# Kernel optimization log

Hardware: AMD Instinct MI355X
Metric: run time of the kernel (lower is better)

## Reference

```python
import jax, jax.numpy as jnp
import numpy as np

N = 10000      # nodes
E = 100000     # edges
C = 32         # in_channels == hidden_channels == out_channels
ED = 4         # edge_dim
G = 64         # number of graphs in the batch
EPS = 1e-5     # BatchNorm eps


def setup_inputs() -> dict:
    key = jax.random.key(0)
    ks = jax.random.split(key, 20)
    rn = lambda k, shape, s=0.05: jax.random.normal(k, shape, dtype=jnp.float32) * s
    return {
        "x": jax.random.normal(ks[0], (N, C), dtype=jnp.float32),
        "edge_attr": jax.random.normal(ks[1], (E, ED), dtype=jnp.float32),
        # edge MLP 1: ED -> C -> C*C ; NNConv1 root/bias
        "e1_w1": rn(ks[2], (ED, C)), "e1_b1": jnp.zeros((C,), jnp.float32),
        "e1_w2": rn(ks[3], (C, C * C)), "e1_b2": jnp.zeros((C * C,), jnp.float32),
        "root1": rn(ks[4], (C, C)), "bias1": jnp.zeros((C,), jnp.float32),
        # edge MLP 2: ED -> C -> C*C ; NNConv2 root/bias
        "e2_w1": rn(ks[5], (ED, C)), "e2_b1": jnp.zeros((C,), jnp.float32),
        "e2_w2": rn(ks[6], (C, C * C)), "e2_b2": jnp.zeros((C * C,), jnp.float32),
        "root2": rn(ks[7], (C, C)), "bias2": jnp.zeros((C,), jnp.float32),
        # BatchNorm (eval mode: running stats)
        "bn1_g": jnp.ones((C,), jnp.float32), "bn1_b": jnp.zeros((C,), jnp.float32),
        "bn1_m": rn(ks[8], (C,), 0.1), "bn1_v": 1.0 + 0.1 * jax.random.uniform(ks[9], (C,), dtype=jnp.float32),
        "bn2_g": jnp.ones((C,), jnp.float32), "bn2_b": jnp.zeros((C,), jnp.float32),
        "bn2_m": rn(ks[10], (C,), 0.1), "bn2_v": 1.0 + 0.1 * jax.random.uniform(ks[11], (C,), dtype=jnp.float32),
        # readout: C -> C//2 -> 1
        "r1_w": rn(ks[12], (C, C // 2)), "r1_b": jnp.zeros((C // 2,), jnp.float32),
        "r2_w": rn(ks[13], (C // 2, 1)), "r2_b": jnp.zeros((1,), jnp.float32),
        "edge_index": jax.random.randint(ks[14], (2, E), 0, N),
        "batch": jnp.sort(jax.random.randint(ks[15], (N,), 0, G)),
    }


def _nnconv(x, edge_index, edge_attr, w1, b1, w2, b2, root, bias):
    # edge MLP -> per-edge weight matrix [E, C, C]
    h = jax.nn.relu(edge_attr @ w1 + b1)
    W = (h @ w2 + b2).reshape(E, C, C)
    src, dst = edge_index[0], edge_index[1]
    # gather source features, per-edge matmul, scatter-mean to target nodes
    msg = jnp.einsum('ei,eio->eo', x[src], W)                      # [E, C]
    agg = jax.ops.segment_sum(msg, dst, num_segments=N)            # [N, C]
    cnt = jax.ops.segment_sum(jnp.ones((E,), x.dtype), dst, num_segments=N)
    agg = agg / jnp.maximum(cnt, 1.0)[:, None]
    return agg + x @ root + bias


def _bn(x, g, b, m, v):
    return (x - m) * jax.lax.rsqrt(v + EPS) * g + b


def reference(x, edge_attr,
              e1_w1, e1_b1, e1_w2, e1_b2, root1, bias1,
              e2_w1, e2_b1, e2_w2, e2_b2, root2, bias2,
              bn1_g, bn1_b, bn1_m, bn1_v,
              bn2_g, bn2_b, bn2_m, bn2_v,
              r1_w, r1_b, r2_w, r2_b,
              edge_index, batch):
    h = jax.nn.relu(_bn(_nnconv(x, edge_index, edge_attr, e1_w1, e1_b1, e1_w2, e1_b2, root1, bias1),
                        bn1_g, bn1_b, bn1_m, bn1_v))
    h = jax.nn.relu(_bn(_nnconv(h, edge_index, edge_attr, e2_w1, e2_b1, e2_w2, e2_b2, root2, bias2),
                        bn2_g, bn2_b, bn2_m, bn2_v))
    # global mean pool over graphs
    psum = jax.ops.segment_sum(h, batch, num_segments=G)           # [G, C]
    pcnt = jax.ops.segment_sum(jnp.ones((N,), h.dtype), batch, num_segments=G)
    pooled = psum / jnp.maximum(pcnt, 1.0)[:, None]
    # readout MLP (dropout is identity in eval)
    return jax.nn.relu(pooled @ r1_w + r1_b) @ r2_w + r2_b          # [G, 1]
```

## Files before the change

kernel.cpp:

```cpp
#include <hip/hip_runtime.h>

#define NN 10000
#define EE 100000
#define CC 32
#define GG 64
#define EPSV 1e-5f
#define NB 8
#define SLOTS 1056
#define PST 36
#define PNODE (32*PST)
#define HBLK ((EE+255)/256)
#define WBLK 160

__global__ __launch_bounds__(256) void k_pre(const int* __restrict__ ei,
        int* __restrict__ cnt, int* __restrict__ deg,
        const float* __restrict__ w2a, const float* __restrict__ b2a,
        const float* __restrict__ w2b, const float* __restrict__ b2b,
        float* __restrict__ w2r1, float* __restrict__ w2r2) {
    int blk = blockIdx.x;
    int t = threadIdx.x;
    if (blk < HBLK) {
        int e = blk * 256 + t;
        if (e < EE) {
            atomicAdd(&cnt[ei[EE + e]], 1);
            atomicAdd(&deg[ei[e]], 1);
        }
    } else {
        int b2i = blk - HBLK;
        int s = (b2i % 5) * 256 + t;
        int i = b2i / 5;
        if (s < SLOTS) {
            float va = (s < 1024) ? w2a[(s >> 5) * 1024 + i * 32 + (s & 31)]
                                  : b2a[i * 32 + (s - 1024)];
            float vb = (s < 1024) ? w2b[(s >> 5) * 1024 + i * 32 + (s & 31)]
                                  : b2b[i * 32 + (s - 1024)];
            w2r1[i * SLOTS + s] = va;
            w2r2[i * SLOTS + s] = vb;
        }
    }
}

__global__ __launch_bounds__(1024) void k_scan(const int* __restrict__ deg,
                                               const int* __restrict__ cnt,
                                               int* __restrict__ rowptr,
                                               int* __restrict__ cursor,
                                               int* __restrict__ colptr,
                                               int* __restrict__ ccursor) {
    __shared__ int buf[1024];
    int t = threadIdx.x;
    int base = t * 10;
    for (int pass = 0; pass < 2; pass++) {
        const int* src = pass ? cnt : deg;
        int* dst_p = pass ? colptr : rowptr;
        int* dst_c = pass ? ccursor : cursor;
        int v[10]; int s = 0;
        #pragma unroll
        for (int k = 0; k < 10; k++) {
            int idx = base + k;
            v[k] = (idx < NN) ? src[idx] : 0;
            s += v[k];
        }
        buf[t] = s;
        for (int off = 1; off < 1024; off <<= 1) {
            __syncthreads();
            int val = buf[t] + ((t >= off) ? buf[t - off] : 0);
            __syncthreads();
            buf[t] = val;
        }
        __syncthreads();
        int carry = (t > 0) ? buf[t - 1] : 0;
        #pragma unroll
        for (int k = 0; k < 10; k++) {
            int idx = base + k;
            if (idx < NN) { dst_p[idx] = carry; dst_c[idx] = carry; }
            carry += v[k];
        }
        if (t == 1023) dst_p[NN] = buf[1023];
        __syncthreads();
    }
}

__global__ void k_scatter(const int* __restrict__ ei,
        const float* __restrict__ edge_attr,
        int* __restrict__ cursor, int* __restrict__ ccursor,
        int* __restrict__ msrc, int* __restrict__ cpos,
        float4* __restrict__ ea_csr) {
    int e = blockIdx.x * 256 + threadIdx.x;
    if (e >= EE) return;
    int sn = ei[e];
    int dn = ei[EE + e];
    float4 a = *(const float4*)&edge_attr[(size_t)e * 4];
    int pos = atomicAdd(&cursor[sn], 1);
    msrc[pos] = sn;
    ea_csr[pos] = a;
    int cp = atomicAdd(&ccursor[dn], 1);
    cpos[cp] = pos;
}

__global__ __launch_bounds__(256, 3) void k_fused3(const float* __restrict__ x,
        const float4* __restrict__ ea_csr,
        const float* __restrict__ w1, const float* __restrict__ b1,
        const float* __restrict__ w2r,
        const int* __restrict__ msrc, const int* __restrict__ rowptr,
        float* __restrict__ msg) {
    __shared__ float xs[NB][32];
    __shared__ float P2[NB * PNODE];
    __shared__ float shx[8][32];
    int t = threadIdx.x;
    int o = t & 31;
    int cb = 4 * (t >> 5);
    int n0 = blockIdx.x * NB;

    int ebase = rowptr[n0];
    int eend  = rowptr[n0 + NB];
    int grp = t >> 5;

    float wc0 = w1[o], wc1 = w1[32 + o], wc2 = w1[64 + o], wc3 = w1[96 + o];
    float bb  = b1[o];

    int pos = ebase + grp;
    float4 aC = make_float4(0.f, 0.f, 0.f, 0.f);
    int srcC = n0;
    if (pos < eend) {
        aC = ea_csr[pos];
        srcC = msrc[pos];
    }

    xs[t >> 5][t & 31] = x[n0 * 32 + t];
    __syncthreads();

    {
        float acc[4][NB];
        #pragma unroll
        for (int k = 0; k < 4; k++)
            #pragma unroll
            for (int n = 0; n < NB; n++) acc[k][n] = 0.f;
        #pragma unroll
        for (int j = 0; j < 8; j++) {
            float wk[4][4];
            #pragma unroll
            for (int r = 0; r < 4; r++)
                #pragma unroll
                for (int k = 0; k < 4; k++)
                    wk[r][k] = w2r[(4 * j + r) * SLOTS + (cb + k) * 32 + o];
            #pragma unroll
            for (int n = 0; n < NB; n++) {
                float4 xq = *(const float4*)&xs[n][4 * j];
                #pragma unroll
                for (int k = 0; k < 4; k++)
                    acc[k][n] += xq.x * wk[0][k] + xq.y * wk[1][k]
                               + xq.z * wk[2][k] + xq.w * wk[3][k];
            }
        }
        #pragma unroll
        for (int n = 0; n < NB; n++) {
            float4 st = make_float4(acc[0][n], acc[1][n], acc[2][n], acc[3][n]);
            *(float4*)&P2[n * PNODE + o * PST + cb] = st;
        }
    }
    if (t < 32) {
        float wb[32];
        #pragma unroll
        for (int i = 0; i < 32; i++) wb[i] = w2r[i * SLOTS + 1024 + t];
        #pragma unroll
        for (int n = 0; n < NB; n++) {
            float b = 0.f;
            #pragma unroll
            for (int j = 0; j < 8; j++) {
                float4 xq = *(const float4*)&xs[n][4 * j];
                b += xq.x * wb[4 * j] + xq.y * wb[4 * j + 1]
                   + xq.z * wb[4 * j + 2] + xq.w * wb[4 * j + 3];
            }
            *(float4*)&P2[n * PNODE + t * PST + 32] = make_float4(b, 0.f, 0.f, 0.f);
        }
    }
    __syncthreads();

    while (pos < eend) {
        int pn = pos + 8;
        float4 aN = aC; int srcN = srcC;
        if (pn < eend) {
            aN = ea_csr[pn];
            srcN = msrc[pn];
        }
        float h = fmaxf(aC.x * wc0 + aC.y * wc1 + aC.z * wc2 + aC.w * wc3 + bb, 0.f);
        shx[grp][o] = h;
        asm volatile("" ::: "memory");
        const float* Pn = &P2[(srcC - n0) * PNODE + o * PST];
        float m = Pn[32];
        #pragma unroll
        for (int b = 0; b < 8; b++) {
            float4 hx = *(const float4*)&shx[grp][4 * b];
            float4 pq = *(const float4*)&Pn[4 * b];
            m += hx.x * pq.x + hx.y * pq.y + hx.z * pq.z + hx.w * pq.w;
        }
        msg[(size_t)pos * 32 + o] = m;
        asm volatile("" ::: "memory");
        pos = pn; aC = aN; srcC = srcN;
    }
}

__global__ __launch_bounds__(256) void k_combine(const float* __restrict__ x_in,
        const float* __restrict__ msg,
        const int* __restrict__ colptr, const int* __restrict__ cpos,
        const float* __restrict__ root, const float* __restrict__ bias,
        const float* __restrict__ bng, const float* __restrict__ bnb,
        const float* __restrict__ bnm, const float* __restrict__ bnv,
        float* __restrict__ x_out, float* __restrict__ psum,
        const int* __restrict__ batch) {
    __shared__ float xs[8][32];
    __shared__ float vals[8][32];
    __shared__ int gb[8];
    int t = threadIdx.x;
    int n0 = blockIdx.x * 8;
    xs[t >> 5][t & 31] = x_in[n0 * 32 + t];
    __syncthreads();
    int k = t >> 5, o = t & 31, n = n0 + k;
    float r = bias[o];
    #pragma unroll
    for (int i = 0; i < 32; i++) r += xs[k][i] * root[i * 32 + o];
    int jbase = colptr[n], jend = colptr[n + 1];
    float acc = 0.f;
    for (int jb = jbase; jb < jend; jb += 32) {
        int nrem = jend - jb;
        int lim = (nrem < 32) ? nrem : 32;
        int cv = 0;
        if (o < lim) cv = cpos[jb + o];
        for (int j = 0; j < lim; j += 8) {
            float v[8];
            #pragma unroll
            for (int q = 0; q < 8; q++) {
                if (j + q < lim) {
                    int cj = __shfl(cv, j + q, 32);
                    v[q] = msg[(size_t)cj * 32 + o];
                } else v[q] = 0.f;
            }
            #pragma unroll
            for (int q = 0; q < 8; q++) acc += v[q];
        }
    }
    float a = acc / fmaxf((float)(jend - jbase), 1.f);
    float val = a + r;
    val = (val - bnm[o]) * rsqrtf(bnv[o] + EPSV) * bng[o] + bnb[o];
    val = fmaxf(val, 0.f);
    if (x_out) {
        x_out[(size_t)n * 32 + o] = val;
    }
    if (psum) {
        vals[k][o] = val;
        if (o == 0) gb[k] = batch[n];
        __syncthreads();
        if (k == 0) {
            float pacc = vals[0][o];
            int g = gb[0];
            #pragma unroll
            for (int k2 = 1; k2 < 8; k2++) {
                if (gb[k2] == g) pacc += vals[k2][o];
                else {
                    atomicAdd(&psum[(size_t)g * 32 + o], pacc);
                    g = gb[k2]; pacc = vals[k2][o];
                }
            }
            atomicAdd(&psum[(size_t)g * 32 + o], pacc);
        }
    }
}

__global__ __launch_bounds__(256) void k_readout(const float* __restrict__ psum,
        const int* __restrict__ batch,
        const float* __restrict__ r1w, const float* __restrict__ r1b,
        const float* __restrict__ r2w, const float* __restrict__ r2b,
        float* __restrict__ out) {
    __shared__ float w1s[32 * 16];
    __shared__ float b1s[16];
    __shared__ float w2s[16];
    __shared__ float ps[GG * 32];
    int t = threadIdx.x;
    int cnt_g = 0;
    if (t < GG) {
        int lo = 0, hi = NN;
        while (lo < hi) { int m = (lo + hi) >> 1; if (batch[m] < t) lo = m + 1; else hi = m; }
        int lb = lo;
        lo = 0; hi = NN;
        while (lo < hi) { int m = (lo + hi) >> 1; if (batch[m] < t + 1) lo = m + 1; else hi = m; }
        cnt_g = lo - lb;
    }
    w1s[t] = r1w[t];
    w1s[t + 256] = r1w[t + 256];
    if (t < 16) { b1s[t] = r1b[t]; w2s[t] = r2w[t]; }
    #pragma unroll
    for (int i = 0; i < GG * 32 / 256; i++) ps[t + i * 256] = psum[t + i * 256];
    __syncthreads();
    if (t < GG) {
        float inv = 1.f / fmaxf((float)cnt_g, 1.f);
        float acc = r2b[0];
        #pragma unroll
        for (int j = 0; j < 16; j++) {
            float dot = 0.f;
            #pragma unroll
            for (int c = 0; c < 32; c++) dot += ps[t * 32 + c] * w1s[c * 16 + j];
            float z = dot * inv + b1s[j];
            acc += fmaxf(z, 0.f) * w2s[j];
        }
        out[t] = acc;
    }
}

extern "C" void kernel_launch(void* const* d_in, const int* in_sizes, int n_in,
                              void* d_out, int out_size, void* d_ws, size_t ws_size,
                              hipStream_t stream) {
    const float* x       = (const float*)d_in[0];
    const float* eattr   = (const float*)d_in[1];
    const float* e1_w1   = (const float*)d_in[2];
    const float* e1_b1   = (const float*)d_in[3];
    const float* e1_w2   = (const float*)d_in[4];
    const float* e1_b2   = (const float*)d_in[5];
    const float* root1   = (const float*)d_in[6];
    const float* bias1   = (const float*)d_in[7];
    const float* e2_w1   = (const float*)d_in[8];
    const float* e2_b1   = (const float*)d_in[9];
    const float* e2_w2   = (const float*)d_in[10];
    const float* e2_b2   = (const float*)d_in[11];
    const float* root2   = (const float*)d_in[12];
    const float* bias2   = (const float*)d_in[13];
    const float* bn1_g   = (const float*)d_in[14];
    const float* bn1_b   = (const float*)d_in[15];
    const float* bn1_m   = (const float*)d_in[16];
    const float* bn1_v   = (const float*)d_in[17];
    const float* bn2_g   = (const float*)d_in[18];
    const float* bn2_b   = (const float*)d_in[19];
    const float* bn2_m   = (const float*)d_in[20];
    const float* bn2_v   = (const float*)d_in[21];
    const float* r1_w    = (const float*)d_in[22];
    const float* r1_b    = (const float*)d_in[23];
    const float* r2_w    = (const float*)d_in[24];
    const float* r2_b    = (const float*)d_in[25];
    const int*   ei      = (const int*)d_in[26];
    const int*   batch   = (const int*)d_in[27];

    char* ws = (char*)d_ws;
    float*  w2r1   = (float*) (ws);
    float*  w2r2   = (float*) (ws + 135168);
    float*  msg    = (float*) (ws + 270336);
    float4* ea_csr = (float4*)(ws + 13070336);
    int*    cnt    = (int*)   (ws + 14670336);
    int*    deg    = (int*)   (ws + 14710336);
    float*  psum   = (float*) (ws + 14750336);
    float*  xmid   = (float*) (ws + 14758528);
    int*    rowptr = (int*)   (ws + 16038528);
    int*    cursor = (int*)   (ws + 16078592);
    int*    colptr = (int*)   (ws + 16118592);
    int*    ccursor= (int*)   (ws + 16158656);
    int*    msrc   = (int*)   (ws + 16198656);
    int*    cpos   = (int*)   (ws + 16598656);

    hipMemsetAsync(ws + 14670336, 0, 88192, stream);

    k_pre<<<HBLK + WBLK, 256, 0, stream>>>(ei, cnt, deg,
                                           e1_w2, e1_b2, e2_w2, e2_b2, w2r1, w2r2);
    k_scan<<<1, 1024, 0, stream>>>(deg, cnt, rowptr, cursor, colptr, ccursor);
    k_scatter<<<(EE + 255) / 256, 256, 0, stream>>>(ei, eattr,
                                                    cursor, ccursor, msrc, cpos,
                                                    ea_csr);

    k_fused3<<<NN / NB, 256, 0, stream>>>(x, ea_csr, e1_w1, e1_b1, w2r1,
                                          msrc, rowptr, msg);
    k_combine<<<NN / 8, 256, 0, stream>>>(x, msg, colptr, cpos, root1, bias1,
                                          bn1_g, bn1_b, bn1_m, bn1_v,
                                          xmid, nullptr, batch);

    k_fused3<<<NN / NB, 256, 0, stream>>>(xmid, ea_csr, e2_w1, e2_b1, w2r2,
                                          msrc, rowptr, msg);
    k_combine<<<NN / 8, 256, 0, stream>>>(xmid, msg, colptr, cpos, root2, bias2,
                                          bn2_g, bn2_b, bn2_m, bn2_v,
                                          nullptr, psum, batch);

    k_readout<<<1, 256, 0, stream>>>(psum, batch, r1_w, r1_b, r2_w, r2_b, (float*)d_out);
}
```

Measured before the change: 255.0 us.

## Fuse all stages into one persistent kernel with software grid barriers

Replaces eight separate kernel launches and a memset with a single 625-block persistent kernel that uses atomic-counter grid barriers between phases: degree counting, scan, CSR scatter, two message/combine layers, and readout. The layer-1 output stays in shared memory for each block's 16 nodes instead of going through global memory, and the two layers write to separate message buffers. The intent is to remove launch overhead and inter-kernel gaps. In exchange it depends on all 625 blocks being co-resident, otherwise the spin barriers deadlock. The scan and readout phases also run on only one or two blocks while the rest wait.

```diff
diff --git a/kernel.cpp b/kernel.cpp
--- a/kernel.cpp
+++ b/kernel.cpp
@@ -2,66 +2,129 @@
 
 #define NN 10000
 #define EE 100000
-#define CC 32
 #define GG 64
 #define EPSV 1e-5f
-#define NB 8
+#define NBLK 625
+#define NPB 16
 #define SLOTS 1056
 #define PST 36
 #define PNODE (32*PST)
-#define HBLK ((EE+255)/256)
+#define HBLK 391
 #define WBLK 160
 
-__global__ __launch_bounds__(256) void k_pre(const int* __restrict__ ei,
-        int* __restrict__ cnt, int* __restrict__ deg,
-        const float* __restrict__ w2a, const float* __restrict__ b2a,
-        const float* __restrict__ w2b, const float* __restrict__ b2b,
-        float* __restrict__ w2r1, float* __restrict__ w2r2) {
-    int blk = blockIdx.x;
-    int t = threadIdx.x;
-    if (blk < HBLK) {
-        int e = blk * 256 + t;
-        if (e < EE) {
-            atomicAdd(&cnt[ei[EE + e]], 1);
-            atomicAdd(&deg[ei[e]], 1);
-        }
-    } else {
-        int b2i = blk - HBLK;
+#define OFF_W2R1   0
+#define OFF_W2R2   135168
+#define OFF_MSG1   270336
+#define OFF_MSG2   13070336
+#define OFF_EACSR  25870336
+#define OFF_CNT    27470336
+#define OFF_DEG    27510336
+#define OFF_PSUM   27550336
+#define OFF_ROWPTR 27558528
+#define OFF_CURSOR 27598592
+#define OFF_COLPTR 27638592
+#define OFF_CCUR   27678656
+#define OFF_MSRC   27718656
+#define OFF_CPOS   28118656
+#define OFF_BARS   28518656
+
+__device__ __forceinline__ void gsync(int* bars, int slot) {
+    __syncthreads();
+    if (threadIdx.x == 0) {
+        __threadfence();
+        int base = atomicAdd(&bars[slot], 1);
+        int target = (base / NBLK + 1) * NBLK;
+        while (__hip_atomic_load(&bars[slot], __ATOMIC_RELAXED,
+                                 __HIP_MEMORY_SCOPE_AGENT) < target)
+            __builtin_amdgcn_s_sleep(2);
+        __threadfence();
+    }
+    __syncthreads();
+}
+
+__global__ __launch_bounds__(256, 3) void k_mega(
+    const float* __restrict__ x, const float* __restrict__ eattr,
+    const float* __restrict__ e1w1, const float* __restrict__ e1b1,
+    const float* __restrict__ e2w1, const float* __restrict__ e2b1,
+    const float* __restrict__ e1w2, const float* __restrict__ e1b2,
+    const float* __restrict__ e2w2, const float* __restrict__ e2b2,
+    const float* __restrict__ root1, const float* __restrict__ bias1,
+    const float* __restrict__ root2, const float* __restrict__ bias2,
+    const float* __restrict__ bn1g, const float* __restrict__ bn1b,
+    const float* __restrict__ bn1m, const float* __restrict__ bn1v,
+    const float* __restrict__ bn2g, const float* __restrict__ bn2b,
+    const float* __restrict__ bn2m, const float* __restrict__ bn2v,
+    const float* __restrict__ r1w, const float* __restrict__ r1b,
+    const float* __restrict__ r2w, const float* __restrict__ r2b,
+    const int* __restrict__ ei, const int* __restrict__ batch,
+    float* __restrict__ out, char* __restrict__ ws)
+{
+    __shared__ float xs[8][32];
+    __shared__ float P2[8 * PNODE];
+    __shared__ float shx[8][32];
+    __shared__ float xmid_s[NPB][32];
+
+    float*  w2r1   = (float*) (ws + OFF_W2R1);
+    float*  w2r2   = (float*) (ws + OFF_W2R2);
+    float*  msg1   = (float*) (ws + OFF_MSG1);
+    float*  msg2   = (float*) (ws + OFF_MSG2);
+    float4* ea_csr = (float4*)(ws + OFF_EACSR);
+    int*    cnt    = (int*)   (ws + OFF_CNT);
+    int*    deg    = (int*)   (ws + OFF_DEG);
+    float*  psum   = (float*) (ws + OFF_PSUM);
+    int*    rowptr = (int*)   (ws + OFF_ROWPTR);
+    int*    cursor = (int*)   (ws + OFF_CURSOR);
+    int*    colptr = (int*)   (ws + OFF_COLPTR);
+    int*    ccursor= (int*)   (ws + OFF_CCUR);
+    int*    msrc   = (int*)   (ws + OFF_MSRC);
+    int*    cpos   = (int*)   (ws + OFF_CPOS);
+    int*    bars   = (int*)   (ws + OFF_BARS);
+
+    int bid  = blockIdx.x;
+    int t    = threadIdx.x;
+    int gtid = bid * 256 + t;
+    int o    = t & 31;
+    int grp  = t >> 5;
+
+    if (gtid < NN) { cnt[gtid] = 0; deg[gtid] = 0; }
+    if (gtid < GG * 32) psum[gtid] = 0.f;
+    if (bid >= HBLK && bid < HBLK + WBLK) {
+        int b2i = bid - HBLK;
         int s = (b2i % 5) * 256 + t;
         int i = b2i / 5;
         if (s < SLOTS) {
-            float va = (s < 1024) ? w2a[(s >> 5) * 1024 + i * 32 + (s & 31)]
-                                  : b2a[i * 32 + (s - 1024)];
-            float vb = (s < 1024) ? w2b[(s >> 5) * 1024 + i * 32 + (s & 31)]
-                                  : b2b[i * 32 + (s - 1024)];
+            float va = (s < 1024) ? e1w2[(s >> 5) * 1024 + i * 32 + (s & 31)]
+                                  : e1b2[i * 32 + (s - 1024)];
+            float vb = (s < 1024) ? e2w2[(s >> 5) * 1024 + i * 32 + (s & 31)]
+                                  : e2b2[i * 32 + (s - 1024)];
             w2r1[i * SLOTS + s] = va;
             w2r2[i * SLOTS + s] = vb;
         }
     }
-}
-
-__global__ __launch_bounds__(1024) void k_scan(const int* __restrict__ deg,
-                                               const int* __restrict__ cnt,
-                                               int* __restrict__ rowptr,
-                                               int* __restrict__ cursor,
-                                               int* __restrict__ colptr,
-                                               int* __restrict__ ccursor) {
-    __shared__ int buf[1024];
-    int t = threadIdx.x;
-    int base = t * 10;
-    for (int pass = 0; pass < 2; pass++) {
-        const int* src = pass ? cnt : deg;
-        int* dst_p = pass ? colptr : rowptr;
-        int* dst_c = pass ? ccursor : cursor;
-        int v[10]; int s = 0;
+    gsync(bars, 0);
+
+    if (gtid < EE) {
+        atomicAdd(&cnt[ei[EE + gtid]], 1);
+        atomicAdd(&deg[ei[gtid]], 1);
+    }
+    gsync(bars, 1);
+
+    if (bid < 2) {
+        const int* srcv = bid ? cnt : deg;
+        int* dp = bid ? colptr : rowptr;
+        int* dc = bid ? ccursor : cursor;
+        int* buf = (int*)xs;
+        int vloc[40];
+        int ssum = 0;
+        int base = t * 40;
         #pragma unroll
-        for (int k = 0; k < 10; k++) {
+        for (int k = 0; k < 40; k++) {
             int idx = base + k;
-            v[k] = (idx < NN) ? src[idx] : 0;
-            s += v[k];
-        }
-        buf[t] = s;
-        for (int off = 1; off < 1024; off <<= 1) {
+            vloc[k] = (idx < NN) ? srcv[idx] : 0;
+            ssum += vloc[k];
+        }
+        buf[t] = ssum;
+        for (int off = 1; off < 256; off <<= 1) {
             __syncthreads();
             int val = buf[t] + ((t >= off) ? buf[t - off] : 0);
             __syncthreads();
@@ -70,239 +133,219 @@
         __syncthreads();
         int carry = (t > 0) ? buf[t - 1] : 0;
         #pragma unroll
-        for (int k = 0; k < 10; k++) {
+        for (int k = 0; k < 40; k++) {
             int idx = base + k;
-            if (idx < NN) { dst_p[idx] = carry; dst_c[idx] = carry; }
-            carry += v[k];
-        }
-        if (t == 1023) dst_p[NN] = buf[1023];
+            if (idx < NN) { dp[idx] = carry; dc[idx] = carry; }
+            carry += vloc[k];
+        }
+        if (t == 255) dp[NN] = buf[255];
+    }
+    gsync(bars, 2);
+
+    if (gtid < EE) {
+        int sn = ei[gtid];
+        int dn = ei[EE + gtid];
+        float4 a = *(const float4*)&eattr[(size_t)gtid * 4];
+        int pos = atomicAdd(&cursor[sn], 1);
+        msrc[pos] = sn;
+        ea_csr[pos] = a;
+        int cp = atomicAdd(&ccursor[dn], 1);
+        cpos[cp] = pos;
+    }
+    gsync(bars, 3);
+
+    for (int layer = 0; layer < 2; ++layer) {
+        const float* w2r  = layer ? w2r2 : w2r1;
+        const float* w1   = layer ? e2w1 : e1w1;
+        const float* b1   = layer ? e2b1 : e1b1;
+        float*       msgL = layer ? msg2 : msg1;
+        const float* root = layer ? root2 : root1;
+        const float* bias = layer ? bias2 : bias1;
+        const float* bg   = layer ? bn2g : bn1g;
+        const float* bbn  = layer ? bn2b : bn1b;
+        const float* bm   = layer ? bn2m : bn1m;
+        const float* bv   = layer ? bn2v : bn1v;
+
+        float wc0 = w1[o], wc1 = w1[32 + o], wc2 = w1[64 + o], wc3 = w1[96 + o];
+        float hbb = b1[o];
+        int cb = 4 * grp;
+
+        for (int tile = 0; tile < 2; ++tile) {
+            int n0 = bid * NPB + tile * 8;
+            int ebase = rowptr[n0];
+            int eend  = rowptr[n0 + 8];
+
+            int pos = ebase + grp;
+            float4 aC = make_float4(0.f, 0.f, 0.f, 0.f);
+            int srcC = n0;
+            if (pos < eend) { aC = ea_csr[pos]; srcC = msrc[pos]; }
+
+            if (layer == 0) xs[grp][o] = x[n0 * 32 + t];
+            else            xs[grp][o] = xmid_s[tile * 8 + grp][o];
+            __syncthreads();
+
+            {
+                float acc[4][8];
+                #pragma unroll
+                for (int k = 0; k < 4; k++)
+                    #pragma unroll
+                    for (int n = 0; n < 8; n++) acc[k][n] = 0.f;
+                #pragma unroll
+                for (int j = 0; j < 8; j++) {
+                    float wk[4][4];
+                    #pragma unroll
+                    for (int r = 0; r < 4; r++)
+                        #pragma unroll
+                        for (int k = 0; k < 4; k++)
+                            wk[r][k] = w2r[(4 * j + r) * SLOTS + (cb + k) * 32 + o];
+                    #pragma unroll
+                    for (int n = 0; n < 8; n++) {
+                        float4 xq = *(const float4*)&xs[n][4 * j];
+                        #pragma unroll
+                        for (int k = 0; k < 4; k++)
+                            acc[k][n] += xq.x * wk[0][k] + xq.y * wk[1][k]
+                                       + xq.z * wk[2][k] + xq.w * wk[3][k];
+                    }
+                }
+                #pragma unroll
+                for (int n = 0; n < 8; n++) {
+                    float4 st = make_float4(acc[0][n], acc[1][n], acc[2][n], acc[3][n]);
+                    *(float4*)&P2[n * PNODE + o * PST + cb] = st;
+                }
+            }
+            if (t < 32) {
+                float wb[32];
+                #pragma unroll
+                for (int i = 0; i < 32; i++) wb[i] = w2r[i * SLOTS + 1024 + t];
+                #pragma unroll
+                for (int n = 0; n < 8; n++) {
+                    float b = 0.f;
+                    #pragma unroll
+                    for (int j = 0; j < 8; j++) {
+                        float4 xq = *(const float4*)&xs[n][4 * j];
+                        b += xq.x * wb[4 * j] + xq.y * wb[4 * j + 1]
+                           + xq.z * wb[4 * j + 2] + xq.w * wb[4 * j + 3];
+                    }
+                    *(float4*)&P2[n * PNODE + t * PST + 32] = make_float4(b, 0.f, 0.f, 0.f);
+                }
+            }
+            __syncthreads();
+
+            while (pos < eend) {
+                int pn = pos + 8;
+                float4 aN = aC; int srcN = srcC;
+                if (pn < eend) { aN = ea_csr[pn]; srcN = msrc[pn]; }
+                float h = fmaxf(aC.x * wc0 + aC.y * wc1 + aC.z * wc2 + aC.w * wc3 + hbb, 0.f);
+                shx[grp][o] = h;
+                asm volatile("" ::: "memory");
+                const float* Pn = &P2[(srcC - n0) * PNODE + o * PST];
+                float m = Pn[32];
+                #pragma unroll
+                for (int b = 0; b < 8; b++) {
+                    float4 hx = *(const float4*)&shx[grp][4 * b];
+                    float4 pq = *(const float4*)&Pn[4 * b];
+                    m += hx.x * pq.x + hx.y * pq.y + hx.z * pq.z + hx.w * pq.w;
+                }
+                msgL[(size_t)pos * 32 + o] = m;
+                asm volatile("" ::: "memory");
+                pos = pn; aC = aN; srcC = srcN;
+            }
+        }
+        gsync(bars, 4 + layer);
+
+        for (int r = 0; r < 2; ++r) {
+            __syncthreads();
+            int n0c = bid * NPB + r * 8;
+            if (layer == 0) xs[grp][o] = x[n0c * 32 + t];
+            else            xs[grp][o] = xmid_s[r * 8 + grp][o];
+            __syncthreads();
+            int k = grp, n = n0c + k;
+            float rt = bias[o];
+            #pragma unroll
+            for (int i = 0; i < 32; i++) rt += xs[k][i] * root[i * 32 + o];
+            int jbase = colptr[n], jend = colptr[n + 1];
+            float acc = 0.f;
+            for (int jb = jbase; jb < jend; jb += 32) {
+                int nrem = jend - jb;
+                int lim = (nrem < 32) ? nrem : 32;
+                int cv = 0;
+                if (o < lim) cv = cpos[jb + o];
+                for (int j = 0; j < lim; j += 8) {
+                    float v[8];
+                    #pragma unroll
+                    for (int q = 0; q < 8; q++) {
+                        if (j + q < lim) {
+                            int cj = __shfl(cv, j + q, 32);
+                            v[q] = msgL[(size_t)cj * 32 + o];
+                        } else v[q] = 0.f;
+                    }
+                    #pragma unroll
+                    for (int q = 0; q < 8; q++) acc += v[q];
+                }
+            }
+            float a = acc / fmaxf((float)(jend - jbase), 1.f);
+            float val = a + rt;
+            val = (val - bm[o]) * rsqrtf(bv[o] + EPSV) * bg[o] + bbn[o];
+            val = fmaxf(val, 0.f);
+            if (layer == 0) {
+                xmid_s[r * 8 + k][o] = val;
+            } else {
+                int* gbp = (int*)P2;
+                shx[k][o] = val;
+                if (o == 0) gbp[k] = batch[n];
+                __syncthreads();
+                if (k == 0) {
+                    float pacc = shx[0][o];
+                    int g = gbp[0];
+                    #pragma unroll
+                    for (int k2 = 1; k2 < 8; k2++) {
+                        if (gbp[k2] == g) pacc += shx[k2][o];
+                        else {
+                            atomicAdd(&psum[(size_t)g * 32 + o], pacc);
+                            g = gbp[k2]; pacc = shx[k2][o];
+                        }
+                    }
+                    atomicAdd(&psum[(size_t)g * 32 + o], pacc);
+                }
+            }
+        }
+        if (layer == 1) gsync(bars, 6);
+    }
+
+    if (bid == 0) {
         __syncthreads();
-    }
-}
-
-__global__ void k_scatter(const int* __restrict__ ei,
-        const float* __restrict__ edge_attr,
-        int* __restrict__ cursor, int* __restrict__ ccursor,
-        int* __restrict__ msrc, int* __restrict__ cpos,
-        float4* __restrict__ ea_csr) {
-    int e = blockIdx.x * 256 + threadIdx.x;
-    if (e >= EE) return;
-    int sn = ei[e];
-    int dn = ei[EE + e];
-    float4 a = *(const float4*)&edge_attr[(size_t)e * 4];
-    int pos = atomicAdd(&cursor[sn], 1);
-    msrc[pos] = sn;
-    ea_csr[pos] = a;
-    int cp = atomicAdd(&ccursor[dn], 1);
-    cpos[cp] = pos;
-}
-
-__global__ __launch_bounds__(256, 3) void k_fused3(const float* __restrict__ x,
-        const float4* __restrict__ ea_csr,
-        const float* __restrict__ w1, const float* __restrict__ b1,
-        const float* __restrict__ w2r,
-        const int* __restrict__ msrc, const int* __restrict__ rowptr,
-        float* __restrict__ msg) {
-    __shared__ float xs[NB][32];
-    __shared__ float P2[NB * PNODE];
-    __shared__ float shx[8][32];
-    int t = threadIdx.x;
-    int o = t & 31;
-    int cb = 4 * (t >> 5);
-    int n0 = blockIdx.x * NB;
-
-    int ebase = rowptr[n0];
-    int eend  = rowptr[n0 + NB];
-    int grp = t >> 5;
-
-    float wc0 = w1[o], wc1 = w1[32 + o], wc2 = w1[64 + o], wc3 = w1[96 + o];
-    float bb  = b1[o];
-
-    int pos = ebase + grp;
-    float4 aC = make_float4(0.f, 0.f, 0.f, 0.f);
-    int srcC = n0;
-    if (pos < eend) {
-        aC = ea_csr[pos];
-        srcC = msrc[pos];
-    }
-
-    xs[t >> 5][t & 31] = x[n0 * 32 + t];
-    __syncthreads();
-
-    {
-        float acc[4][NB];
+        float* w1s = P2;
+        float* b1s = P2 + 512;
+        float* w2s = P2 + 528;
+        float* ps  = P2 + 544;
+        int cnt_g = 0;
+        if (t < GG) {
+            int lo = 0, hi = NN;
+            while (lo < hi) { int m2 = (lo + hi) >> 1; if (batch[m2] < t) lo = m2 + 1; else hi = m2; }
+            int lb = lo;
+            lo = 0; hi = NN;
+            while (lo < hi) { int m2 = (lo + hi) >> 1; if (batch[m2] < t + 1) lo = m2 + 1; else hi = m2; }
+            cnt_g = lo - lb;
+        }
+        w1s[t] = r1w[t];
+        w1s[t + 256] = r1w[t + 256];
+        if (t < 16) { b1s[t] = r1b[t]; w2s[t] = r2w[t]; }
         #pragma unroll
-        for (int k = 0; k < 4; k++)
+        for (int i = 0; i < GG * 32 / 256; i++) ps[t + i * 256] = psum[t + i * 256];
+        __syncthreads();
+        if (t < GG) {
+            float inv = 1.f / fmaxf((float)cnt_g, 1.f);
+            float acc2 = r2b[0];
             #pragma unroll
-            for (int n = 0; n < NB; n++) acc[k][n] = 0.f;
-        #pragma unroll
-        for (int j = 0; j < 8; j++) {
-            float wk[4][4];
-            #pragma unroll
-            for (int r = 0; r < 4; r++)
-                #pragma unroll
-                for (int k = 0; k < 4; k++)
-                    wk[r][k] = w2r[(4 * j + r) * SLOTS + (cb + k) * 32 + o];
-            #pragma unroll
-            for (int n = 0; n < NB; n++) {
-                float4 xq = *(const float4*)&xs[n][4 * j];
-                #pragma unroll
-                for (int k = 0; k < 4; k++)
-                    acc[k][n] += xq.x * wk[0][k] + xq.y * wk[1][k]
-                               + xq.z * wk[2][k] + xq.w * wk[3][k];
-            }
-        }
-        #pragma unroll
-        for (int n = 0; n < NB; n++) {
-            float4 st = make_float4(acc[0][n], acc[1][n], acc[2][n], acc[3][n]);
-            *(float4*)&P2[n * PNODE + o * PST + cb] = st;
-        }
-    }
-    if (t < 32) {
-        float wb[32];
-        #pragma unroll
-        for (int i = 0; i < 32; i++) wb[i] = w2r[i * SLOTS + 1024 + t];
-        #pragma unroll
-        for (int n = 0; n < NB; n++) {
-            float b = 0.f;
-            #pragma unroll
-            for (int j = 0; j < 8; j++) {
-                float4 xq = *(const float4*)&xs[n][4 * j];
-                b += xq.x * wb[4 * j] + xq.y * wb[4 * j + 1]
-                   + xq.z * wb[4 * j + 2] + xq.w * wb[4 * j + 3];
-            }
-            *(float4*)&P2[n * PNODE + t * PST + 32] = make_float4(b, 0.f, 0.f, 0.f);
-        }
-    }
-    __syncthreads();
-
-    while (pos < eend) {
-        int pn = pos + 8;
-        float4 aN = aC; int srcN = srcC;
-        if (pn < eend) {
-            aN = ea_csr[pn];
-            srcN = msrc[pn];
-        }
-        float h = fmaxf(aC.x * wc0 + aC.y * wc1 + aC.z * wc2 + aC.w * wc3 + bb, 0.f);
-        shx[grp][o] = h;
-        asm volatile("" ::: "memory");
-        const float* Pn = &P2[(srcC - n0) * PNODE + o * PST];
-        float m = Pn[32];
-        #pragma unroll
-        for (int b = 0; b < 8; b++) {
-            float4 hx = *(const float4*)&shx[grp][4 * b];
-            float4 pq = *(const float4*)&Pn[4 * b];
-            m += hx.x * pq.x + hx.y * pq.y + hx.z * pq.z + hx.w * pq.w;
-        }
-        msg[(size_t)pos * 32 + o] = m;
-        asm volatile("" ::: "memory");
-        pos = pn; aC = aN; srcC = srcN;
-    }
-}
-
-__global__ __launch_bounds__(256) void k_combine(const float* __restrict__ x_in,
-        const float* __restrict__ msg,
-        const int* __restrict__ colptr, const int* __restrict__ cpos,
-        const float* __restrict__ root, const float* __restrict__ bias,
-        const float* __restrict__ bng, const float* __restrict__ bnb,
-        const float* __restrict__ bnm, const float* __restrict__ bnv,
-        float* __restrict__ x_out, float* __restrict__ psum,
-        const int* __restrict__ batch) {
-    __shared__ float xs[8][32];
-    __shared__ float vals[8][32];
-    __shared__ int gb[8];
-    int t = threadIdx.x;
-    int n0 = blockIdx.x * 8;
-    xs[t >> 5][t & 31] = x_in[n0 * 32 + t];
-    __syncthreads();
-    int k = t >> 5, o = t & 31, n = n0 + k;
-    float r = bias[o];
-    #pragma unroll
-    for (int i = 0; i < 32; i++) r += xs[k][i] * root[i * 32 + o];
-    int jbase = colptr[n], jend = colptr[n + 1];
-    float acc = 0.f;
-    for (int jb = jbase; jb < jend; jb += 32) {
-        int nrem = jend - jb;
-        int lim = (nrem < 32) ? nrem : 32;
-        int cv = 0;
-        if (o < lim) cv = cpos[jb + o];
-        for (int j = 0; j < lim; j += 8) {
-            float v[8];
-            #pragma unroll
-            for (int q = 0; q < 8; q++) {
-                if (j + q < lim) {
-                    int cj = __shfl(cv, j + q, 32);
-                    v[q] = msg[(size_t)cj * 32 + o];
-                } else v[q] = 0.f;
-            }
-            #pragma unroll
-            for (int q = 0; q < 8; q++) acc += v[q];
-        }
-    }
-    float a = acc / fmaxf((float)(jend - jbase), 1.f);
-    float val = a + r;
-    val = (val - bnm[o]) * rsqrtf(bnv[o] + EPSV) * bng[o] + bnb[o];
-    val = fmaxf(val, 0.f);
-    if (x_out) {
-        x_out[(size_t)n * 32 + o] = val;
-    }
-    if (psum) {
-        vals[k][o] = val;
-        if (o == 0) gb[k] = batch[n];
-        __syncthreads();
-        if (k == 0) {
-            float pacc = vals[0][o];
-            int g = gb[0];
-            #pragma unroll
-            for (int k2 = 1; k2 < 8; k2++) {
-                if (gb[k2] == g) pacc += vals[k2][o];
-                else {
-                    atomicAdd(&psum[(size_t)g * 32 + o], pacc);
-                    g = gb[k2]; pacc = vals[k2][o];
-                }
-            }
-            atomicAdd(&psum[(size_t)g * 32 + o], pacc);
-        }
-    }
-}
-
-__global__ __launch_bounds__(256) void k_readout(const float* __restrict__ psum,
-        const int* __restrict__ batch,
-        const float* __restrict__ r1w, const float* __restrict__ r1b,
-        const float* __restrict__ r2w, const float* __restrict__ r2b,
-        float* __restrict__ out) {
-    __shared__ float w1s[32 * 16];
-    __shared__ float b1s[16];
-    __shared__ float w2s[16];
-    __shared__ float ps[GG * 32];
-    int t = threadIdx.x;
-    int cnt_g = 0;
-    if (t < GG) {
-        int lo = 0, hi = NN;
-        while (lo < hi) { int m = (lo + hi) >> 1; if (batch[m] < t) lo = m + 1; else hi = m; }
-        int lb = lo;
-        lo = 0; hi = NN;
-        while (lo < hi) { int m = (lo + hi) >> 1; if (batch[m] < t + 1) lo = m + 1; else hi = m; }
-        cnt_g = lo - lb;
-    }
-    w1s[t] = r1w[t];
-    w1s[t + 256] = r1w[t + 256];
-    if (t < 16) { b1s[t] = r1b[t]; w2s[t] = r2w[t]; }
-    #pragma unroll
-    for (int i = 0; i < GG * 32 / 256; i++) ps[t + i * 256] = psum[t + i * 256];
-    __syncthreads();
-    if (t < GG) {
-        float inv = 1.f / fmaxf((float)cnt_g, 1.f);
-        float acc = r2b[0];
-        #pragma unroll
-        for (int j = 0; j < 16; j++) {
-            float dot = 0.f;
-            #pragma unroll
-            for (int c = 0; c < 32; c++) dot += ps[t * 32 + c] * w1s[c * 16 + j];
-            float z = dot * inv + b1s[j];
-            acc += fmaxf(z, 0.f) * w2s[j];
-        }
-        out[t] = acc;
+            for (int j = 0; j < 16; j++) {
+                float dot = 0.f;
+                #pragma unroll
+                for (int c = 0; c < 32; c++) dot += ps[t * 32 + c] * w1s[c * 16 + j];
+                float z = dot * inv + b1s[j];
+                acc2 += fmaxf(z, 0.f) * w2s[j];
+            }
+            out[t] = acc2;
+        }
     }
 }
 
@@ -339,41 +382,16 @@
     const int*   batch   = (const int*)d_in[27];
 
     char* ws = (char*)d_ws;
-    float*  w2r1   = (float*) (ws);
-    float*  w2r2   = (float*) (ws + 135168);
-    float*  msg    = (float*) (ws + 270336);
-    float4* ea_csr = (float4*)(ws + 13070336);
-    int*    cnt    = (int*)   (ws + 14670336);
-    int*    deg    = (int*)   (ws + 14710336);
-    float*  psum   = (float*) (ws + 14750336);
-    float*  xmid   = (float*) (ws + 14758528);
-    int*    rowptr = (int*)   (ws + 16038528);
-    int*    cursor = (int*)   (ws + 16078592);
-    int*    colptr = (int*)   (ws + 16118592);
-    int*    ccursor= (int*)   (ws + 16158656);
-    int*    msrc   = (int*)   (ws + 16198656);
-    int*    cpos   = (int*)   (ws + 16598656);
-
-    hipMemsetAsync(ws + 14670336, 0, 88192, stream);
-
-    k_pre<<<HBLK + WBLK, 256, 0, stream>>>(ei, cnt, deg,
-                                           e1_w2, e1_b2, e2_w2, e2_b2, w2r1, w2r2);
-    k_scan<<<1, 1024, 0, stream>>>(deg, cnt, rowptr, cursor, colptr, ccursor);
-    k_scatter<<<(EE + 255) / 256, 256, 0, stream>>>(ei, eattr,
-                                                    cursor, ccursor, msrc, cpos,
-                                                    ea_csr);
-
-    k_fused3<<<NN / NB, 256, 0, stream>>>(x, ea_csr, e1_w1, e1_b1, w2r1,
-                                          msrc, rowptr, msg);
-    k_combine<<<NN / 8, 256, 0, stream>>>(x, msg, colptr, cpos, root1, bias1,
-                                          bn1_g, bn1_b, bn1_m, bn1_v,
-                                          xmid, nullptr, batch);
-
-    k_fused3<<<NN / NB, 256, 0, stream>>>(xmid, ea_csr, e2_w1, e2_b1, w2r2,
-                                          msrc, rowptr, msg);
-    k_combine<<<NN / 8, 256, 0, stream>>>(xmid, msg, colptr, cpos, root2, bias2,
-                                          bn2_g, bn2_b, bn2_m, bn2_v,
-                                          nullptr, psum, batch);
-
-    k_readout<<<1, 256, 0, stream>>>(psum, batch, r1_w, r1_b, r2_w, r2_b, (float*)d_out);
+
+    hipMemsetAsync(ws + OFF_BARS, 0, 64, stream);
+
+    k_mega<<<NBLK, 256, 0, stream>>>(
+        x, eattr,
+        e1_w1, e1_b1, e2_w1, e2_b1,
+        e1_w2, e1_b2, e2_w2, e2_b2,
+        root1, bias1, root2, bias2,
+        bn1_g, bn1_b, bn1_m, bn1_v,
+        bn2_g, bn2_b, bn2_m, bn2_v,
+        r1_w, r1_b, r2_w, r2_b,
+        ei, batch, (float*)d_out, ws);
 }
```

After: 997.8 us. +291.3%, slower.
